# Kernel optimization log

Measured on AMD Instinct MI355X. Metric: run time of the kernel, lower is better.

The kernel has to match this reference:

```python
import jax, jax.numpy as jnp
import numpy as np

N_SEGMENT = 8   # frames per clip (init arg n_segment)
P = 4           # patch_size (init arg)
EPS = 1e-5      # torch F.layer_norm default eps


def setup_inputs() -> dict:
    key = jax.random.key(0)
    # (b*t, c, h, w) = (16*8, 256, 28, 28)
    x = jax.random.normal(key, (128, 256, 28, 28), dtype=jnp.float32)
    return {"x": x}


def _layer_norm(x):
    # F.layer_norm over last dim, no affine params
    m = jnp.mean(x, axis=-1, keepdims=True)
    v = jnp.var(x, axis=-1, keepdims=True)
    return (x - m) * jax.lax.rsqrt(v + EPS)


def _self_attention(x):
    # q = k = v = x; scores = softmax(q k^T / sqrt(E)); out = scores @ v
    e = x.shape[-1]
    scores = jnp.einsum('bqe,bke->bqk', x, x) * (1.0 / float(np.sqrt(e)))
    scores = jax.nn.softmax(scores, axis=-1)
    return jnp.einsum('bqk,bke->bqe', scores, x)


def reference(x):
    t, p = N_SEGMENT, P
    bt, c, h, w = x.shape
    b = bt // t
    ph, pw = h // p, w // p
    e = p * p * c  # patch embedding dim = 4096

    # rearrange '(b t) c (ph p1) (pw p2) -> (b ph pw) t (p1 p2 c)'
    y = x.reshape(b, t, c, ph, p, pw, p)
    y = y.transpose(0, 3, 5, 1, 4, 6, 2).reshape(b * ph * pw, t, e)

    # temporal: layernorm + shift-left-diff + self-attention + residual
    xn = _layer_norm(y)
    xn = jnp.concatenate([xn[:, 1:], jnp.zeros_like(xn[:, :1])], axis=1) - xn
    y = _self_attention(xn) + y

    # rearrange '(b ph pw) t e -> (b t) (ph pw) e'
    y = y.reshape(b, ph, pw, t, e).transpose(0, 3, 1, 2, 4).reshape(b * t, ph * pw, e)

    # spatial: layernorm + self-attention + residual
    xn = _layer_norm(y)
    y = _self_attention(xn) + y

    # rearrange '(b t) (ph pw) (p1 p2 c) -> (b t) c (ph p1) (pw p2)'
    y = y.reshape(b, t, ph, pw, p, p, c)
    y = y.transpose(0, 1, 6, 2, 4, 3, 5).reshape(bt, c, h, w)
    return y
```

## Files before the change

### kernel.cpp

```cpp
#include <hip/hip_runtime.h>


#define IDX36(a,b) ((((a)*8)+(b))-((((a)*((a)+1)))/2))
#define YP 4128

typedef __attribute__((ext_vector_type(8)))  short bf16x8;
typedef __attribute__((ext_vector_type(16))) float f32x16;

__device__ __forceinline__ float wsum64(float v){
  #pragma unroll
  for (int off=32; off; off>>=1) v += __shfl_xor(v, off);
  return v;
}
__device__ __forceinline__ float wsum32(float v){
  #pragma unroll
  for (int off=16; off; off>>=1) v += __shfl_xor(v, off);
  return v;
}
__device__ __forceinline__ unsigned int rne_bf16(float f){
  unsigned int b = __float_as_uint(f);
  return (b + 0x7FFFu + ((b>>16)&1u)) >> 16;
}

__global__ __launch_bounds__(256) void k_t1(const float* __restrict__ x, float* __restrict__ wsG){
  const int bx = blockIdx.x;
  const int b = bx / 112;
  const int ph = (bx % 112) / 16;
  const int slice = bx & 15;
  const int c0 = slice * 16;
  const int tid = threadIdx.x;

  __shared__ float lds[8*16*116];
  const float4* x4 = reinterpret_cast<const float4*>(x);

  #pragma unroll
  for (int t=0;t<8;t++){
    const int base = ((b*8+t)*256 + c0)*196 + ph*28;
    {
      const int f = tid, c = f/28, m = f%28;
      *reinterpret_cast<float4*>(&lds[(t*16+c)*116 + m*4]) = x4[base + c*196 + m];
    }
    if (tid < 192){
      const int f = 256+tid, c = f/28, m = f%28;
      *reinterpret_cast<float4*>(&lds[(t*16+c)*116 + m*4]) = x4[base + c*196 + m];
    }
  }
  __syncthreads();

  const int pw   = tid >> 5;
  const int slot = tid & 31;
  const int c    = slot >> 1;
  const int p1b  = (slot & 1) * 2;

  float v[8][8];
  #pragma unroll
  for (int t=0;t<8;t++){
    const float* p = &lds[(t*16+c)*116 + p1b*28 + pw*4];
    const float4 a  = *reinterpret_cast<const float4*>(p);
    const float4 b2 = *reinterpret_cast<const float4*>(p + 28);
    v[t][0]=a.x;  v[t][1]=a.y;  v[t][2]=a.z;  v[t][3]=a.w;
    v[t][4]=b2.x; v[t][5]=b2.y; v[t][6]=b2.z; v[t][7]=b2.w;
  }

  float Au[36], sm[8];
  #pragma unroll
  for (int a2=0;a2<8;a2++){
    float s0 = 0.f;
    #pragma unroll
    for (int e=0;e<8;e++) s0 += v[a2][e];
    sm[a2] = s0;
    #pragma unroll
    for (int b2=a2;b2<8;b2++){
      float s = 0.f;
      #pragma unroll
      for (int e=0;e<8;e++) s += v[a2][e]*v[b2][e];
      Au[IDX36(a2,b2)] = s;
    }
  }
  #pragma unroll
  for (int i=0;i<36;i++) Au[i] = wsum32(Au[i]);
  #pragma unroll
  for (int t=0;t<8;t++) sm[t] = wsum32(sm[t]);

  if (slot == 0 && pw < 7){
    const int base = ((b*49 + ph*7 + pw)*16 + slice)*44;
    #pragma unroll
    for (int i=0;i<36;i++) wsG[base+i] = Au[i];
    #pragma unroll
    for (int t=0;t<8;t++)  wsG[base+36+t] = sm[t];
  }
}

__global__ __launch_bounds__(64) void k_t2(const float* __restrict__ wsG, float* __restrict__ wsWt){
  const int seq = blockIdx.x;
  const int lane = threadIdx.x;
  __shared__ float red[44];
  if (lane < 44){
    float a = 0.f;
    #pragma unroll
    for (int s=0;s<16;s++) a += wsG[(seq*16+s)*44 + lane];
    red[lane] = a;
  }
  __syncthreads();
  if (lane < 8){
    const int i = lane;
    float Ar[36], mean[8], rstd[8];
    #pragma unroll
    for (int k=0;k<36;k++) Ar[k] = red[k];
    #pragma unroll
    for (int t=0;t<8;t++){
      const float sv = red[36+t];
      mean[t] = sv * (1.f/4096.f);
      const float var = Ar[IDX36(t,t)] * (1.f/4096.f) - mean[t]*mean[t];
      rstd[t] = rsqrtf(var + 1e-5f);
    }
    #define GV(a,b) ((((a)<8)&&((b)<8)) ? (rstd[(a)]*rstd[(b)]*(Ar[((a)<=(b))?IDX36((a),(b)):IDX36((b),(a))] - 4096.f*mean[(a)]*mean[(b)])) : 0.f)
    float l[8]; float mx = -1e30f;
    #pragma unroll
    for (int j=0;j<8;j++){
      const float sij = GV(i+1,j+1) - GV(i+1,j) - GV(i,j+1) + GV(i,j);
      l[j] = sij * (1.f/64.f);
      mx = fmaxf(mx, l[j]);
    }
    float ss = 0.f;
    #pragma unroll
    for (int j=0;j<8;j++){ l[j] = __expf(l[j]-mx); ss += l[j]; }
    const float inv = 1.f/ss;
    float cc = 0.f;
    #pragma unroll
    for (int k2=0;k2<8;k2++){
      const float q = (((k2>=1)? l[k2-1] : 0.f) - l[k2]) * inv;
      const float wv2 = q * rstd[k2];
      wsWt[seq*72 + i*8 + k2] = wv2;
      cc -= wv2 * mean[k2];
    }
    wsWt[seq*72 + 64 + i] = cc;
    #undef GV
  }
}

__global__ __launch_bounds__(256) void k_t3(const float* __restrict__ x, const float* __restrict__ wsWt,
                                            unsigned short* __restrict__ y1u){
  const int bx = blockIdx.x;
  const int b = bx / 112;
  const int ph = (bx % 112) / 16;
  const int slice = bx & 15;
  const int c0 = slice * 16;
  const int tid = threadIdx.x;

  __shared__ float Wl[7][72];
  for (int idx=tid; idx<504; idx+=256)
    Wl[idx/72][idx%72] = wsWt[(b*49 + ph*7 + idx/72)*72 + idx%72];
  __syncthreads();

  const float4* x4 = reinterpret_cast<const float4*>(x);

  #pragma unroll
  for (int fi=0; fi<2; fi++){
    const int f = fi*256 + tid;
    if (f < 448){
      const int c = f/28, m = f%28, pw = m%7, p1 = m/7;
      float4 v[8];
      #pragma unroll
      for (int t=0;t<8;t++) v[t] = x4[((b*8+t)*256 + c0+c)*196 + ph*28 + m];
      const float* W = Wl[pw];
      const int pp = ph*7 + pw;
      #pragma unroll
      for (int i=0;i<8;i++){
        const float ci = W[64+i];
        float4 o;
        o.x = v[i].x + ci; o.y = v[i].y + ci; o.z = v[i].z + ci; o.w = v[i].w + ci;
        #pragma unroll
        for (int j=0;j<8;j++){
          const float w = W[i*8+j];
          o.x += w*v[j].x; o.y += w*v[j].y; o.z += w*v[j].z; o.w += w*v[j].w;
        }
        const unsigned int h0=rne_bf16(o.x), h1=rne_bf16(o.y), h2=rne_bf16(o.z), h3=rne_bf16(o.w);
        const size_t ybase = (size_t)((b*8+i)*49 + pp)*YP + (c0+c)*16 + p1*4;
        *reinterpret_cast<uint2*>(&y1u[ybase]) = make_uint2(h0|(h1<<16), h2|(h3<<16));
      }
    }
  }
}

__global__ __launch_bounds__(256,3) void k_s1(const unsigned short* __restrict__ y1u, float* __restrict__ wsA){
  const int bt = blockIdx.x >> 2;
  const int slice = blockIdx.x & 3;
  const int tid = threadIdx.x;
  const int wave = tid >> 6, lane = tid & 63;

  __shared__ unsigned short Ah[64*136];
  __shared__ float red[64*52];
  for (int i=tid; i<64*52; i+=256) red[i] = 0.f;

  for (int idx=tid; idx<15*128; idx+=256){
    const int rr = 49 + idx/128, cc = idx%128;
    Ah[rr*136 + cc] = (rr==49) ? (unsigned short)0x3F80 : (unsigned short)0;
  }

  f32x16 acc00, acc01, acc11;
  #pragma unroll
  for (int i=0;i<16;i++){ acc00[i]=0.f; acc01[i]=0.f; acc11[i]=0.f; }

  const int r0 = lane & 31;
  const int koff = (lane >> 5) * 8;
  const int lrow = tid >> 4;
  const int lq   = tid & 15;

#define ISSUE(pf, ch) { \
  _Pragma("unroll") \
  for (int p=0;p<4;p++){ \
    const int row = p*16 + lrow; \
    pf[p] = make_uint4(0u,0u,0u,0u); \
    if (row < 49) pf[p] = *reinterpret_cast<const uint4*>(&y1u[(size_t)(bt*49+row)*YP + slice*1024 + (ch)*128 + lq*8]); } }

#define CW(pf) { \
  _Pragma("unroll") \
  for (int p=0;p<4;p++){ \
    const int row = p*16 + lrow; \
    if (row < 49) *reinterpret_cast<uint4*>(&Ah[row*136 + lq*8]) = pf[p]; } }

#define MF() { \
  _Pragma("unroll") \
  for (int kk=0;kk<2;kk++){ \
    const int kw = (wave + kk*4)*16; \
    const bf16x8 f0 = *reinterpret_cast<const bf16x8*>(&Ah[ r0     *136 + kw + koff]); \
    const bf16x8 f1 = *reinterpret_cast<const bf16x8*>(&Ah[(32+r0)*136 + kw + koff]); \
    acc00 = __builtin_amdgcn_mfma_f32_32x32x16_bf16(f0, f0, acc00, 0,0,0); \
    acc01 = __builtin_amdgcn_mfma_f32_32x32x16_bf16(f0, f1, acc01, 0,0,0); \
    acc11 = __builtin_amdgcn_mfma_f32_32x32x16_bf16(f1, f1, acc11, 0,0,0); } }

  uint4 pfA[4], pfB[4];
  ISSUE(pfA, 0);
  #pragma unroll
  for (int ch=0; ch<8; ch+=2){
    if (ch+1<8) ISSUE(pfB, ch+1);
    __syncthreads();
    CW(pfA);
    __syncthreads();
    MF();
    if (ch+2<8) ISSUE(pfA, ch+2);
    __syncthreads();
    CW(pfB);
    __syncthreads();
    MF();
  }
  __syncthreads();

  const int ccol = lane & 31;
  const int rbase = 4*(lane>>5);
  #pragma unroll
  for (int q2=0;q2<16;q2++){
    const int rr = (q2&3) + 8*(q2>>2) + rbase;
    atomicAdd(&red[ rr    *52 + ccol     ], acc00[q2]);
    atomicAdd(&red[ rr    *52 + 32 + ccol], acc01[q2]);
    atomicAdd(&red[(rr+32)*52 + 32 + ccol], acc11[q2]);
  }
  __syncthreads();
  float* wp = wsA + blockIdx.x * 2500;
  for (int idx=tid; idx<2500; idx+=256){
    const int i2 = idx/50, j2 = idx%50;
    wp[idx] = (i2>=32 && j2<32) ? red[j2*52+i2] : red[i2*52+j2];
  }
#undef ISSUE
#undef CW
#undef MF
}

__global__ __launch_bounds__(256) void k_s2(const float* __restrict__ wsA, float* __restrict__ wsWT, float* __restrict__ wsC){
  const int bt = blockIdx.x;
  const int tid = threadIdx.x;
  __shared__ float A[2500];
  __shared__ float m[49], r[49];
  for (int idx=tid; idx<2548; idx+=256) wsWT[bt*2548+idx] = 0.f;
  for (int idx=tid; idx<2500; idx+=256){
    float v = 0.f;
    #pragma unroll
    for (int sl=0; sl<4; sl++) v += wsA[(bt*4+sl)*2500 + idx];
    A[idx] = v;
  }
  __syncthreads();
  if (tid < 49){
    const float mm = A[49*50+tid] * (1.f/4096.f);
    const float var = A[tid*50+tid] * (1.f/4096.f) - mm*mm;
    m[tid]=mm; r[tid]=rsqrtf(var+1e-5f);
  }
  __syncthreads();
  const int wv = tid>>6, lane = tid&63;
  for (int i=wv; i<49; i+=4){
    const float ri = r[i], mi = m[i];
    float rv=0.f, mv=0.f, L=-1e30f;
    if (lane < 49){
      rv = r[lane]; mv = m[lane];
      L = ri*rv*(A[i*50+lane] - 4096.f*mi*mv) * (1.f/64.f);
    }
    float mx = L;
    #pragma unroll
    for (int off=32; off; off>>=1) mx = fmaxf(mx, __shfl_xor(mx, off));
    const float p = (lane<49) ? __expf(L-mx) : 0.f;
    const float ss = wsum64(p);
    const float Wv = (p/ss)*rv;
    if (lane < 49) wsWT[bt*2548 + lane*52 + i] = Wv + ((lane==i) ? 1.f : 0.f);
    const float cp = wsum64(-Wv*mv);
    if (lane == 0) wsC[bt*49+i] = cp;
  }
}

__global__ __launch_bounds__(256,2) void k_s3(const unsigned short* __restrict__ y1u, const float* __restrict__ wsWT,
                                              const float* __restrict__ wsC, float* __restrict__ out){
  const int bt = blockIdx.x >> 3;
  const int chunk = blockIdx.x & 7;
  const int tid = threadIdx.x;
  const int wave = tid >> 6, lane = tid & 63;

  __shared__ unsigned short Wh[64*68], Wlo[64*68];
  for (int idx=tid; idx<64*64; idx+=256){
    const int i = idx>>6, j = idx&63;
    float v = 0.f;
    if (i < 49){
      if (j < 49)       v = wsWT[bt*2548 + j*52 + i];
      else if (j == 49) v = wsC[bt*49 + i];
    }
    const unsigned int u = __float_as_uint(v);
    Wh [i*68+j] = (unsigned short)(u>>16);
    Wlo[i*68+j] = (unsigned short)rne_bf16(v - __uint_as_float(u & 0xFFFF0000u));
  }
  __syncthreads();

  const int r0 = lane & 31;
  const int koff = (lane >> 5) * 8;
  bf16x8 A0h[4], A0l[4], A1h[4], A1l[4];
  #pragma unroll
  for (int kk=0;kk<4;kk++){
    const int off = kk*16 + koff;
    A0h[kk] = *reinterpret_cast<const bf16x8*>(&Wh [ r0     *68 + off]);
    A0l[kk] = *reinterpret_cast<const bf16x8*>(&Wlo[ r0     *68 + off]);
    A1h[kk] = *reinterpret_cast<const bf16x8*>(&Wh [(32+r0)*68 + off]);
    A1l[kk] = *reinterpret_cast<const bf16x8*>(&Wlo[(32+r0)*68 + off]);
  }

  const unsigned short* ybu = y1u + (size_t)bt*49*YP;
  float* ob_base = out + bt*200704;
  const bool lo32 = (lane < 32);

  #pragma unroll
  for (int tt=0; tt<4; tt++){
    const int ecol = chunk*512 + (wave*4+tt)*32 + r0;
    const unsigned short* pb = ybu + (size_t)koff*YP + ecol;

    f32x16 acc0, acc1;
    #pragma unroll
    for (int i=0;i<16;i++){ acc0[i]=0.f; acc1[i]=0.f; }

    #pragma unroll
    for (int kk=0;kk<4;kk++){
      bf16x8 Bh;
      if (kk < 3){
        #pragma unroll
        for (int s=0;s<8;s++)
          Bh[s] = (short)pb[(size_t)(kk*16+s)*YP];
      } else {
        const unsigned short h48 = lo32 ? pb[(size_t)48*YP] : (unsigned short)0;
        Bh[0] = (short)h48;
        Bh[1] = lo32 ? (short)0x3F80 : (short)0;
        #pragma unroll
        for (int s=2;s<8;s++) Bh[s]=0;
      }
      acc0 = __builtin_amdgcn_mfma_f32_32x32x16_bf16(A0h[kk], Bh, acc0, 0,0,0);
      acc0 = __builtin_amdgcn_mfma_f32_32x32x16_bf16(A0l[kk], Bh, acc0, 0,0,0);
      acc1 = __builtin_amdgcn_mfma_f32_32x32x16_bf16(A1h[kk], Bh, acc1, 0,0,0);
      acc1 = __builtin_amdgcn_mfma_f32_32x32x16_bf16(A1l[kk], Bh, acc1, 0,0,0);
    }

    const int c  = ecol >> 4;
    const int p1 = (ecol >> 2) & 3;
    const int p2 = ecol & 3;
    float* ob = ob_base + c*784 + p1*28 + p2;
    const int rbase = 4*(lane>>5);
    #pragma unroll
    for (int q=0;q<16;q++){
      const int i0 = (q&3) + 8*(q>>2) + rbase;
      ob[(i0/7)*112 + (i0%7)*4] = acc0[q];
      const int i1 = 32 + i0;
      if (i1 < 49) ob[(i1/7)*112 + (i1%7)*4] = acc1[q];
    }
  }
}

extern "C" void kernel_launch(void* const* d_in, const int* in_sizes, int n_in,
                              void* d_out, int out_size, void* d_ws, size_t ws_size,
                              hipStream_t stream) {
  const float* x = (const float*)d_in[0];
  float* out = (float*)d_out;
  float* ws  = (float*)d_ws;
  unsigned short* y1u = (unsigned short*)ws;
  float* wsA  = ws + 13000000;
  float* wsWT = wsA + 512*2500;
  float* wsC  = wsWT + 128*2548;
  float* wsG  = wsA;
  float* wsWt = wsA + 551936;
  hipLaunchKernelGGL(k_t1, dim3(1792), dim3(256), 0, stream, x, wsG);
  hipLaunchKernelGGL(k_t2, dim3(784),  dim3(64),  0, stream, wsG, wsWt);
  hipLaunchKernelGGL(k_t3, dim3(1792), dim3(256), 0, stream, x, wsWt, y1u);
  hipLaunchKernelGGL(k_s1, dim3(512),  dim3(256), 0, stream, y1u, wsA);
  hipLaunchKernelGGL(k_s2, dim3(128),  dim3(256), 0, stream, wsA, wsWT, wsC);
  hipLaunchKernelGGL(k_s3, dim3(1024), dim3(256), 0, stream, y1u, wsWT, wsC, out);
}
```

Before: 182.9 us.

## Drop bf16 split precision in spatial output GEMM and pair columns per lane

The final spatial-attention apply kernel stops splitting the weight matrix into high and low bf16 parts and uses a single RNE bf16 copy, which halves its MFMA count and LDS footprint. Each lane now loads two adjacent bf16 columns with one 32-bit load and writes float2 pairs, widening global accesses. The launch-bounds occupancy hint rises from 2 to 3 blocks per SM. Rounding the attention weights, including the identity residual term, to bf16 lowers accuracy and may push results past tolerance.

```diff
diff --git a/kernel.cpp b/kernel.cpp
--- a/kernel.cpp
+++ b/kernel.cpp
@@ -306,14 +306,14 @@
   }
 }
 
-__global__ __launch_bounds__(256,2) void k_s3(const unsigned short* __restrict__ y1u, const float* __restrict__ wsWT,
+__global__ __launch_bounds__(256,3) void k_s3(const unsigned short* __restrict__ y1u, const float* __restrict__ wsWT,
                                               const float* __restrict__ wsC, float* __restrict__ out){
   const int bt = blockIdx.x >> 3;
   const int chunk = blockIdx.x & 7;
   const int tid = threadIdx.x;
   const int wave = tid >> 6, lane = tid & 63;
 
-  __shared__ unsigned short Wh[64*68], Wlo[64*68];
+  __shared__ unsigned short Wh[64*68];
   for (int idx=tid; idx<64*64; idx+=256){
     const int i = idx>>6, j = idx&63;
     float v = 0.f;
@@ -321,22 +321,18 @@
       if (j < 49)       v = wsWT[bt*2548 + j*52 + i];
       else if (j == 49) v = wsC[bt*49 + i];
     }
-    const unsigned int u = __float_as_uint(v);
-    Wh [i*68+j] = (unsigned short)(u>>16);
-    Wlo[i*68+j] = (unsigned short)rne_bf16(v - __uint_as_float(u & 0xFFFF0000u));
+    Wh[i*68+j] = (unsigned short)rne_bf16(v);
   }
   __syncthreads();
 
   const int r0 = lane & 31;
   const int koff = (lane >> 5) * 8;
-  bf16x8 A0h[4], A0l[4], A1h[4], A1l[4];
+  bf16x8 A0h[4], A1h[4];
   #pragma unroll
   for (int kk=0;kk<4;kk++){
     const int off = kk*16 + koff;
-    A0h[kk] = *reinterpret_cast<const bf16x8*>(&Wh [ r0     *68 + off]);
-    A0l[kk] = *reinterpret_cast<const bf16x8*>(&Wlo[ r0     *68 + off]);
-    A1h[kk] = *reinterpret_cast<const bf16x8*>(&Wh [(32+r0)*68 + off]);
-    A1l[kk] = *reinterpret_cast<const bf16x8*>(&Wlo[(32+r0)*68 + off]);
+    A0h[kk] = *reinterpret_cast<const bf16x8*>(&Wh[ r0     *68 + off]);
+    A1h[kk] = *reinterpret_cast<const bf16x8*>(&Wh[(32+r0)*68 + off]);
   }
 
   const unsigned short* ybu = y1u + (size_t)bt*49*YP;
@@ -344,45 +340,51 @@
   const bool lo32 = (lane < 32);
 
   #pragma unroll
-  for (int tt=0; tt<4; tt++){
-    const int ecol = chunk*512 + (wave*4+tt)*32 + r0;
-    const unsigned short* pb = ybu + (size_t)koff*YP + ecol;
-
-    f32x16 acc0, acc1;
-    #pragma unroll
-    for (int i=0;i<16;i++){ acc0[i]=0.f; acc1[i]=0.f; }
+  for (int pt=0; pt<2; pt++){
+    const int ecol0 = chunk*512 + (wave*2+pt)*64;
+    const unsigned short* pb = ybu + (size_t)koff*YP + ecol0 + 2*r0;
+
+    f32x16 acc0A, acc0B, acc1A, acc1B;
+    #pragma unroll
+    for (int i=0;i<16;i++){ acc0A[i]=0.f; acc0B[i]=0.f; acc1A[i]=0.f; acc1B[i]=0.f; }
 
     #pragma unroll
     for (int kk=0;kk<4;kk++){
-      bf16x8 Bh;
+      bf16x8 BA, BB;
       if (kk < 3){
         #pragma unroll
-        for (int s=0;s<8;s++)
-          Bh[s] = (short)pb[(size_t)(kk*16+s)*YP];
+        for (int s=0;s<8;s++){
+          const unsigned int u = *reinterpret_cast<const unsigned int*>(&pb[(size_t)(kk*16+s)*YP]);
+          BA[s] = (short)(u & 0xFFFFu);
+          BB[s] = (short)(u >> 16);
+        }
       } else {
-        const unsigned short h48 = lo32 ? pb[(size_t)48*YP] : (unsigned short)0;
-        Bh[0] = (short)h48;
-        Bh[1] = lo32 ? (short)0x3F80 : (short)0;
+        const unsigned int u48 = lo32 ? *reinterpret_cast<const unsigned int*>(&pb[(size_t)48*YP]) : 0u;
+        BA[0] = (short)(u48 & 0xFFFFu);  BB[0] = (short)(u48 >> 16);
+        BA[1] = lo32 ? (short)0x3F80 : (short)0;
+        BB[1] = lo32 ? (short)0x3F80 : (short)0;
         #pragma unroll
-        for (int s=2;s<8;s++) Bh[s]=0;
+        for (int s=2;s<8;s++){ BA[s]=0; BB[s]=0; }
       }
-      acc0 = __builtin_amdgcn_mfma_f32_32x32x16_bf16(A0h[kk], Bh, acc0, 0,0,0);
-      acc0 = __builtin_amdgcn_mfma_f32_32x32x16_bf16(A0l[kk], Bh, acc0, 0,0,0);
-      acc1 = __builtin_amdgcn_mfma_f32_32x32x16_bf16(A1h[kk], Bh, acc1, 0,0,0);
-      acc1 = __builtin_amdgcn_mfma_f32_32x32x16_bf16(A1l[kk], Bh, acc1, 0,0,0);
-    }
-
-    const int c  = ecol >> 4;
-    const int p1 = (ecol >> 2) & 3;
-    const int p2 = ecol & 3;
+      acc0A = __builtin_amdgcn_mfma_f32_32x32x16_bf16(A0h[kk], BA, acc0A, 0,0,0);
+      acc0B = __builtin_amdgcn_mfma_f32_32x32x16_bf16(A0h[kk], BB, acc0B, 0,0,0);
+      acc1A = __builtin_amdgcn_mfma_f32_32x32x16_bf16(A1h[kk], BA, acc1A, 0,0,0);
+      acc1B = __builtin_amdgcn_mfma_f32_32x32x16_bf16(A1h[kk], BB, acc1B, 0,0,0);
+    }
+
+    const int eA = ecol0 + 2*r0;
+    const int c  = eA >> 4;
+    const int p1 = (eA >> 2) & 3;
+    const int p2 = eA & 3;
     float* ob = ob_base + c*784 + p1*28 + p2;
     const int rbase = 4*(lane>>5);
     #pragma unroll
     for (int q=0;q<16;q++){
       const int i0 = (q&3) + 8*(q>>2) + rbase;
-      ob[(i0/7)*112 + (i0%7)*4] = acc0[q];
+      *reinterpret_cast<float2*>(ob + (i0/7)*112 + (i0%7)*4) = make_float2(acc0A[q], acc0B[q]);
       const int i1 = 32 + i0;
-      if (i1 < 49) ob[(i1/7)*112 + (i1%7)*4] = acc1[q];
+      if (i1 < 49)
+        *reinterpret_cast<float2*>(ob + (i1/7)*112 + (i1%7)*4) = make_float2(acc1A[q], acc1B[q]);
     }
   }
 }
```

New measurement: 185.4 us. About the same (+1.4%).
